# Optimization experiments

Measured on AMD Instinct MI355X. Metric: run time of the kernel, lower is better.

## Reference

```python
import jax, jax.numpy as jnp
import numpy as np

H = 256      # hidden_size (hardcoded by view([-1,1,256]) in the torch source)
V = 50257    # output_size / vocab
L = 50       # max_length


def gru_cell(x, h, w_ih, w_hh, b_ih, b_hh):
    """PyTorch GRUCell semantics. x, h: [H]; w_*: [3H, H]; b_*: [3H]."""
    gi = w_ih @ x + b_ih
    gh = w_hh @ h + b_hh
    gi_r, gi_z, gi_n = jnp.split(gi, 3)
    gh_r, gh_z, gh_n = jnp.split(gh, 3)
    r = jax.nn.sigmoid(gi_r + gh_r)
    z = jax.nn.sigmoid(gi_z + gh_z)
    n = jnp.tanh(gi_n + r * gh_n)
    return (1.0 - z) * n + z * h


def setup_inputs() -> dict:
    key = jax.random.key(0)
    ks = jax.random.split(key, 24)
    p = lambda k, shape: (0.02 * jax.random.normal(k, shape)).astype(jnp.float32)
    d = {}
    d["token"] = jax.random.randint(ks[0], (1,), 0, V)
    d["hidden"] = jax.random.normal(ks[1], (1, 1, H), dtype=jnp.float32)
    d["encoder_outputs"] = jax.random.normal(ks[2], (L, H), dtype=jnp.float32)
    d["emb"] = p(ks[3], (V, H))
    d["attn_W"] = p(ks[4], (L, 2 * H)); d["attn_b"] = jnp.zeros((L,), jnp.float32)
    d["comb_W"] = p(ks[5], (H, 2 * H)); d["comb_b"] = jnp.zeros((H,), jnp.float32)
    # bidirectional GRU: forward (f) and reverse (b) direction weights
    d["w_ih_f"] = p(ks[6], (3 * H, H)); d["w_hh_f"] = p(ks[7], (3 * H, H))
    d["b_ih_f"] = jnp.zeros((3 * H,), jnp.float32); d["b_hh_f"] = jnp.zeros((3 * H,), jnp.float32)
    d["w_ih_b"] = p(ks[8], (3 * H, H)); d["w_hh_b"] = p(ks[9], (3 * H, H))
    d["b_ih_b"] = jnp.zeros((3 * H,), jnp.float32); d["b_hh_b"] = jnp.zeros((3 * H,), jnp.float32)
    # second (unidirectional) GRU
    d["w_ih_g"] = p(ks[10], (3 * H, H)); d["w_hh_g"] = p(ks[11], (3 * H, H))
    d["b_ih_g"] = jnp.zeros((3 * H,), jnp.float32); d["b_hh_g"] = jnp.zeros((3 * H,), jnp.float32)
    d["out_W"] = p(ks[12], (V, H)); d["out_b"] = jnp.zeros((V,), jnp.float32)
    return d


def reference(token, hidden, encoder_outputs, emb, attn_W, attn_b, comb_W, comb_b,
              w_ih_f, w_hh_f, b_ih_f, b_hh_f, w_ih_b, w_hh_b, b_ih_b, b_hh_b,
              w_ih_g, w_hh_g, b_ih_g, b_hh_g, out_W, out_b):
    # dropout is treated as identity (eval mode)
    e = emb[token[0]]                       # [H] embedded token
    h0 = hidden[0, 0]                       # [H]
    # attention weights over encoder positions
    aw = jax.nn.softmax(jax.nn.relu(attn_W @ jnp.concatenate([e, h0]) + attn_b))  # [L]
    applied = aw @ encoder_outputs          # [H]
    x = jax.nn.relu(comb_W @ jnp.concatenate([e, applied]) + comb_b)              # [H]
    # bidirectional GRU, seq_len=1: both directions see the same step, init hidden = h0
    hf = gru_cell(x, h0, w_ih_f, w_hh_f, b_ih_f, b_hh_f)
    hb = gru_cell(x, h0, w_ih_b, w_hh_b, b_ih_b, b_hh_b)
    hm = 0.5 * (hf + hb)                    # torch.mean(bihidden, dim=0)
    # bioutput (1,1,512) viewed as (2,1,256) -> second GRU runs 2 steps
    h1 = gru_cell(hf, hm, w_ih_g, w_hh_g, b_ih_g, b_hh_g)
    h2 = gru_cell(hb, h1, w_ih_g, w_hh_g, b_ih_g, b_hh_g)
    logp = jax.nn.log_softmax(out_W @ h1 + out_b)  # output[0] = first timestep = h1
    return (logp[None, :], h2[None, None, :], aw[None, :])
```

## Files before the change

### kernel.cpp

```cpp
#include <hip/hip_runtime.h>
#include <math.h>

#define H 256
#define L 50
#define V 50257
#define LOGIT_BLKS 786
#define ROWS_PER_WAVE 16
#define FINAL_BLKS 197
#define GRU2_BLKS 64

__device__ __forceinline__ float dot4(float4 a, float4 b) {
    return a.x * b.x + a.y * b.y + a.z * b.z + a.w * b.w;
}

__device__ __forceinline__ float wave_reduce_sum(float v) {
#pragma unroll
    for (int m = 32; m >= 1; m >>= 1) v += __shfl_xor(v, m, 64);
    return v;
}

__device__ __forceinline__ float wave_reduce_max(float v) {
#pragma unroll
    for (int m = 32; m >= 1; m >>= 1) v = fmaxf(v, __shfl_xor(v, m, 64));
    return v;
}

__device__ __forceinline__ float sigmoidf(float x) { return 1.0f / (1.0f + __expf(-x)); }

__device__ __forceinline__ void ms_push(float& m, float& s, float x) {
    float mn = fmaxf(m, x);
    s = s * __expf(m - mn) + __expf(x - mn);
    m = mn;
}
__device__ __forceinline__ void ms_merge(float& m, float& s, float om, float os) {
    float M = fmaxf(m, om);
    float a = (m == -INFINITY) ? 0.f : s * __expf(m - M);
    float c = (om == -INFINITY) ? 0.f : os * __expf(om - M);
    m = M; s = a + c;
}

__device__ __forceinline__ void gru_wave(
    int j, int lane, float4 xv, float4 hv, float hj,
    const float* __restrict__ w_ih, const float* __restrict__ w_hh,
    const float* __restrict__ b_ih, const float* __restrict__ b_hh,
    float* __restrict__ outp)
{
    float gi[3], gh[3];
#pragma unroll
    for (int k = 0; k < 3; ++k) {
        int row = k * H + j;
        const float4* wi4 = (const float4*)(w_ih + (size_t)row * H);
        const float4* wh4 = (const float4*)(w_hh + (size_t)row * H);
        gi[k] = wave_reduce_sum(dot4(wi4[lane], xv)) + b_ih[row];
        gh[k] = wave_reduce_sum(dot4(wh4[lane], hv)) + b_hh[row];
    }
    if (lane == 0) {
        float r = sigmoidf(gi[0] + gh[0]);
        float z = sigmoidf(gi[1] + gh[1]);
        float n = tanhf(gi[2] + r * gh[2]);
        outp[j] = (1.f - z) * n + z * hj;
    }
}

__global__ __launch_bounds__(256) void k_comb(
    const int* __restrict__ token, const float* __restrict__ hidden,
    const float* __restrict__ emb, const float* __restrict__ attn_W,
    const float* __restrict__ attn_b, const float* __restrict__ enc,
    const float* __restrict__ comb_W, const float* __restrict__ comb_b,
    float* __restrict__ ws_x, float* __restrict__ out_aw)
{
    __shared__ __align__(16) float s_cat[2 * H];
    __shared__ float s_aw[64];
    int t = threadIdx.x, wid = t >> 6, lane = t & 63;
    int tok = token[0];
    s_cat[t] = emb[(size_t)tok * H + t];
    s_cat[H + t] = hidden[t];
    __syncthreads();
    const float4* c4 = (const float4*)s_cat;
    float4 cA = c4[lane];
    float4 cB = c4[lane + 64];
    for (int r = wid; r < L; r += 4) {
        const float4* W4 = (const float4*)(attn_W + (size_t)r * 2 * H);
        float acc = dot4(W4[lane], cA) + dot4(W4[lane + 64], cB);
        acc = wave_reduce_sum(acc);
        if (lane == 0) s_aw[r] = fmaxf(acc + attn_b[r], 0.f);
    }
    __syncthreads();
    if (t < 64) {
        float v = (t < L) ? s_aw[t] : -INFINITY;
        float mx = wave_reduce_max(v);
        float e = (t < L) ? __expf(v - mx) : 0.f;
        float ssum = wave_reduce_sum(e);
        if (t < L) {
            float aw = e / ssum;
            s_aw[t] = aw;
            if (blockIdx.x == 0) out_aw[t] = aw;
        }
    }
    __syncthreads();
    float app = 0.f;
    for (int l = 0; l < L; ++l) app += s_aw[l] * enc[l * H + t];
    s_cat[H + t] = app;
    __syncthreads();
    int row = blockIdx.x * 4 + wid;
    const float4* Wc = (const float4*)(comb_W + (size_t)row * 2 * H);
    float4 cB2 = c4[lane + 64];
    float acc = dot4(Wc[lane], cA) + dot4(Wc[lane + 64], cB2);
    acc = wave_reduce_sum(acc);
    if (lane == 0) ws_x[row] = fmaxf(acc + comb_b[row], 0.f);
}

__global__ __launch_bounds__(256) void k_gru_fb(
    const float* __restrict__ ws_x, const float* __restrict__ hidden,
    const float* __restrict__ w_ih_f, const float* __restrict__ w_hh_f,
    const float* __restrict__ b_ih_f, const float* __restrict__ b_hh_f,
    const float* __restrict__ w_ih_b, const float* __restrict__ w_hh_b,
    const float* __restrict__ b_ih_b, const float* __restrict__ b_hh_b,
    float* __restrict__ ws_hf, float* __restrict__ ws_hb)
{
    int t = threadIdx.x, wid = t >> 6, lane = t & 63;
    int g = blockIdx.x * 4 + wid;
    int dir = g >> 8, j = g & 255;
    gru_wave(j, lane, ((const float4*)ws_x)[lane], ((const float4*)hidden)[lane],
             hidden[j],
             dir ? w_ih_b : w_ih_f, dir ? w_hh_b : w_hh_f,
             dir ? b_ih_b : b_ih_f, dir ? b_hh_b : b_hh_f,
             dir ? ws_hb : ws_hf);
}

__global__ __launch_bounds__(256) void k_gru(
    const float* __restrict__ xvec, const float* __restrict__ ha,
    const float* __restrict__ hb,
    const float* __restrict__ w_ih, const float* __restrict__ w_hh,
    const float* __restrict__ b_ih, const float* __restrict__ b_hh,
    float* __restrict__ outp)
{
    int t = threadIdx.x, wid = t >> 6, lane = t & 63;
    int j = blockIdx.x * 4 + wid;
    float4 xv = ((const float4*)xvec)[lane];
    float4 hv = ((const float4*)ha)[lane];
    float hj;
    if (hb) {
        float4 bv = ((const float4*)hb)[lane];
        hv = make_float4(0.5f * (hv.x + bv.x), 0.5f * (hv.y + bv.y),
                         0.5f * (hv.z + bv.z), 0.5f * (hv.w + bv.w));
        hj = 0.5f * (ha[j] + hb[j]);
    } else {
        hj = ha[j];
    }
    gru_wave(j, lane, xv, hv, hj, w_ih, w_hh, b_ih, b_hh, outp);
}

__global__ __launch_bounds__(256) void k_logits(
    const float* __restrict__ out_W, const float* __restrict__ out_b,
    const float* __restrict__ h1, float* __restrict__ logits,
    float* __restrict__ part_m, float* __restrict__ part_s)
{
    __shared__ float s_m4[4], s_s4[4];
    int t = threadIdx.x, wid = t >> 6, lane = t & 63;
    float4 hv = ((const float4*)h1)[lane];
    int base = (blockIdx.x * 4 + wid) * ROWS_PER_WAVE;
    float m = -INFINITY, s = 0.f;
#pragma unroll 1
    for (int k = 0; k < ROWS_PER_WAVE; k += 2) {
        int v = base + k;
        if (v >= V) break;
        const float4* W0 = (const float4*)(out_W + (size_t)v * H);
        float4 a0 = W0[lane];
        bool has2 = (v + 1 < V);
        float4 a1 = has2 ? ((const float4*)(out_W + (size_t)(v + 1) * H))[lane]
                         : make_float4(0.f, 0.f, 0.f, 0.f);
        float x0 = wave_reduce_sum(dot4(a0, hv)) + out_b[v];
        float x1 = wave_reduce_sum(dot4(a1, hv));
        if (lane == 0) logits[v] = x0;
        ms_push(m, s, x0);
        if (has2) {
            x1 += out_b[v + 1];
            if (lane == 0) logits[v + 1] = x1;
            ms_push(m, s, x1);
        }
    }
    if (lane == 0) { s_m4[wid] = m; s_s4[wid] = s; }
    __syncthreads();
    if (t == 0) {
        float M = s_m4[0], S = s_s4[0];
#pragma unroll
        for (int q = 1; q < 4; ++q) ms_merge(M, S, s_m4[q], s_s4[q]);
        part_m[blockIdx.x] = M; part_s[blockIdx.x] = S;
    }
}

__global__ __launch_bounds__(256) void k_final(
    const float* __restrict__ part_m, const float* __restrict__ part_s,
    float* __restrict__ logits,
    const float* __restrict__ h1, const float* __restrict__ hb,
    const float* __restrict__ w_ih_g, const float* __restrict__ w_hh_g,
    const float* __restrict__ b_ih_g, const float* __restrict__ b_hh_g,
    float* __restrict__ out_h2)
{
    int t = threadIdx.x, wid = t >> 6, lane = t & 63;
    if (blockIdx.x >= FINAL_BLKS) {
        int j = (blockIdx.x - FINAL_BLKS) * 4 + wid;
        gru_wave(j, lane, ((const float4*)hb)[lane], ((const float4*)h1)[lane],
                 h1[j], w_ih_g, w_hh_g, b_ih_g, b_hh_g, out_h2);
        return;
    }
    __shared__ float s_m4[4], s_s4[4];
    __shared__ float s_bcast;
    float m = -INFINITY, s = 0.f;
    for (int idx = t; idx < LOGIT_BLKS; idx += 256)
        ms_merge(m, s, part_m[idx], part_s[idx]);
#pragma unroll
    for (int d = 32; d >= 1; d >>= 1) {
        float om = __shfl_xor(m, d, 64);
        float os = __shfl_xor(s, d, 64);
        ms_merge(m, s, om, os);
    }
    if (lane == 0) { s_m4[wid] = m; s_s4[wid] = s; }
    __syncthreads();
    if (t == 0) {
        float M = s_m4[0], S = s_s4[0];
#pragma unroll
        for (int q = 1; q < 4; ++q) ms_merge(M, S, s_m4[q], s_s4[q]);
        s_bcast = M + logf(S);
    }
    __syncthreads();
    float lse = s_bcast;
    int i = blockIdx.x * 256 + t;
    if (i < V) logits[i] -= lse;
}

extern "C" void kernel_launch(void* const* d_in, const int* in_sizes, int n_in,
                              void* d_out, int out_size, void* d_ws, size_t ws_size,
                              hipStream_t stream)
{
    const int*   token  = (const int*)d_in[0];
    const float* hidden = (const float*)d_in[1];
    const float* enc    = (const float*)d_in[2];
    const float* emb    = (const float*)d_in[3];
    const float* attn_W = (const float*)d_in[4];
    const float* attn_b = (const float*)d_in[5];
    const float* comb_W = (const float*)d_in[6];
    const float* comb_b = (const float*)d_in[7];
    const float* w_ih_f = (const float*)d_in[8];
    const float* w_hh_f = (const float*)d_in[9];
    const float* b_ih_f = (const float*)d_in[10];
    const float* b_hh_f = (const float*)d_in[11];
    const float* w_ih_b = (const float*)d_in[12];
    const float* w_hh_b = (const float*)d_in[13];
    const float* b_ih_b = (const float*)d_in[14];
    const float* b_hh_b = (const float*)d_in[15];
    const float* w_ih_g = (const float*)d_in[16];
    const float* w_hh_g = (const float*)d_in[17];
    const float* b_ih_g = (const float*)d_in[18];
    const float* b_hh_g = (const float*)d_in[19];
    const float* out_W  = (const float*)d_in[20];
    const float* out_b  = (const float*)d_in[21];

    float* out = (float*)d_out;
    float* ws  = (float*)d_ws;
    float* ws_x      = ws;
    float* ws_hf     = ws + 256;
    float* ws_hb     = ws + 512;
    float* ws_h1     = ws + 768;
    float* part_m    = ws + 1024;
    float* part_s    = ws + 1856;

    k_comb<<<64, 256, 0, stream>>>(token, hidden, emb, attn_W, attn_b, enc,
                                   comb_W, comb_b, ws_x, out + V + H);
    k_gru_fb<<<128, 256, 0, stream>>>(ws_x, hidden,
                                      w_ih_f, w_hh_f, b_ih_f, b_hh_f,
                                      w_ih_b, w_hh_b, b_ih_b, b_hh_b,
                                      ws_hf, ws_hb);
    k_gru<<<64, 256, 0, stream>>>(ws_hf, ws_hf, ws_hb,
                                  w_ih_g, w_hh_g, b_ih_g, b_hh_g, ws_h1);
    k_logits<<<LOGIT_BLKS, 256, 0, stream>>>(out_W, out_b, ws_h1, out,
                                             part_m, part_s);
    k_final<<<FINAL_BLKS + GRU2_BLKS, 256, 0, stream>>>(
        part_m, part_s, out, ws_h1, ws_hb,
        w_ih_g, w_hh_g, b_ih_g, b_hh_g, out + V);
}
```

Before: 182.3 us.

## Fuse attention, GRU stages and logits into one kernel with flag-based inter-block sync

Merges the combine, bidirectional GRU, first second-GRU step and logits kernels into a single launch. Block ranges are assigned to each stage, and dependent blocks spin on per-block release/acquire flags in the workspace instead of waiting for kernel boundaries. Logit blocks prefetch most of their out_W rows into registers before waiting for h1, so the weight streaming overlaps the serial GRU chain. Flags are set to a fixed magic value and never cleared, so if the workspace persists across calls, later calls can read stale intermediates. The spin-waits also depend on producer blocks being resident together with the waiting blocks.

New measurement: 447.2 us. 145% more time.

```diff
diff --git a/kernel.cpp b/kernel.cpp
--- a/kernel.cpp
+++ b/kernel.cpp
@@ -4,10 +4,23 @@
 #define H 256
 #define L 50
 #define V 50257
-#define LOGIT_BLKS 786
-#define ROWS_PER_WAVE 16
+#define MAGIC 0x5F3C7A19u
+
+#define COMB_NB 64
+#define FB_B0   64
+#define FB_NB   128
+#define G1_B0   192
+#define G1_NB   64
+#define SW_B0   256
+#define SW_NB   640
+#define NBLK1   (SW_B0 + SW_NB)
+#define ROWS    20
+#define HOLD    12
+#define NPART   SW_NB
+
 #define FINAL_BLKS 197
-#define GRU2_BLKS 64
+#define H2_NB      64
+#define NBLK2      (FINAL_BLKS + H2_NB)
 
 __device__ __forceinline__ float dot4(float4 a, float4 b) {
     return a.x * b.x + a.y * b.y + a.z * b.z + a.w * b.w;
@@ -26,6 +39,19 @@
 }
 
 __device__ __forceinline__ float sigmoidf(float x) { return 1.0f / (1.0f + __expf(-x)); }
+
+__device__ __forceinline__ void st_flag(unsigned* p, unsigned v) {
+    __hip_atomic_store(p, v, __ATOMIC_RELEASE, __HIP_MEMORY_SCOPE_AGENT);
+}
+__device__ __forceinline__ unsigned ld_flag(const unsigned* p) {
+    return __hip_atomic_load(p, __ATOMIC_ACQUIRE, __HIP_MEMORY_SCOPE_AGENT);
+}
+__device__ __forceinline__ void st_f(float* p, float v) {
+    __hip_atomic_store(p, v, __ATOMIC_RELAXED, __HIP_MEMORY_SCOPE_AGENT);
+}
+__device__ __forceinline__ float ld_f(const float* p) {
+    return __hip_atomic_load(p, __ATOMIC_RELAXED, __HIP_MEMORY_SCOPE_AGENT);
+}
 
 __device__ __forceinline__ void ms_push(float& m, float& s, float x) {
     float mn = fmaxf(m, x);
@@ -58,135 +84,171 @@
         float r = sigmoidf(gi[0] + gh[0]);
         float z = sigmoidf(gi[1] + gh[1]);
         float n = tanhf(gi[2] + r * gh[2]);
-        outp[j] = (1.f - z) * n + z * hj;
-    }
-}
-
-__global__ __launch_bounds__(256) void k_comb(
+        st_f(outp + j, (1.f - z) * n + z * hj);
+    }
+}
+
+__global__ __launch_bounds__(256, 4) void k_fused(
     const int* __restrict__ token, const float* __restrict__ hidden,
-    const float* __restrict__ emb, const float* __restrict__ attn_W,
-    const float* __restrict__ attn_b, const float* __restrict__ enc,
+    const float* __restrict__ enc, const float* __restrict__ emb,
+    const float* __restrict__ attn_W, const float* __restrict__ attn_b,
     const float* __restrict__ comb_W, const float* __restrict__ comb_b,
-    float* __restrict__ ws_x, float* __restrict__ out_aw)
-{
-    __shared__ __align__(16) float s_cat[2 * H];
-    __shared__ float s_aw[64];
-    int t = threadIdx.x, wid = t >> 6, lane = t & 63;
-    int tok = token[0];
-    s_cat[t] = emb[(size_t)tok * H + t];
-    s_cat[H + t] = hidden[t];
-    __syncthreads();
-    const float4* c4 = (const float4*)s_cat;
-    float4 cA = c4[lane];
-    float4 cB = c4[lane + 64];
-    for (int r = wid; r < L; r += 4) {
-        const float4* W4 = (const float4*)(attn_W + (size_t)r * 2 * H);
-        float acc = dot4(W4[lane], cA) + dot4(W4[lane + 64], cB);
-        acc = wave_reduce_sum(acc);
-        if (lane == 0) s_aw[r] = fmaxf(acc + attn_b[r], 0.f);
-    }
-    __syncthreads();
-    if (t < 64) {
-        float v = (t < L) ? s_aw[t] : -INFINITY;
-        float mx = wave_reduce_max(v);
-        float e = (t < L) ? __expf(v - mx) : 0.f;
-        float ssum = wave_reduce_sum(e);
-        if (t < L) {
-            float aw = e / ssum;
-            s_aw[t] = aw;
-            if (blockIdx.x == 0) out_aw[t] = aw;
-        }
-    }
-    __syncthreads();
-    float app = 0.f;
-    for (int l = 0; l < L; ++l) app += s_aw[l] * enc[l * H + t];
-    s_cat[H + t] = app;
-    __syncthreads();
-    int row = blockIdx.x * 4 + wid;
-    const float4* Wc = (const float4*)(comb_W + (size_t)row * 2 * H);
-    float4 cB2 = c4[lane + 64];
-    float acc = dot4(Wc[lane], cA) + dot4(Wc[lane + 64], cB2);
-    acc = wave_reduce_sum(acc);
-    if (lane == 0) ws_x[row] = fmaxf(acc + comb_b[row], 0.f);
-}
-
-__global__ __launch_bounds__(256) void k_gru_fb(
-    const float* __restrict__ ws_x, const float* __restrict__ hidden,
     const float* __restrict__ w_ih_f, const float* __restrict__ w_hh_f,
     const float* __restrict__ b_ih_f, const float* __restrict__ b_hh_f,
     const float* __restrict__ w_ih_b, const float* __restrict__ w_hh_b,
     const float* __restrict__ b_ih_b, const float* __restrict__ b_hh_b,
-    float* __restrict__ ws_hf, float* __restrict__ ws_hb)
+    const float* __restrict__ w_ih_g, const float* __restrict__ w_hh_g,
+    const float* __restrict__ b_ih_g, const float* __restrict__ b_hh_g,
+    const float* __restrict__ out_W, const float* __restrict__ out_b,
+    float* __restrict__ out_logp, float* __restrict__ out_aw,
+    float* __restrict__ ws_x, float* __restrict__ ws_hf,
+    float* __restrict__ ws_hb, float* __restrict__ ws_h1,
+    float* __restrict__ part_m, float* __restrict__ part_s,
+    unsigned* __restrict__ flags)
 {
+    __shared__ float smem[576];
     int t = threadIdx.x, wid = t >> 6, lane = t & 63;
-    int g = blockIdx.x * 4 + wid;
-    int dir = g >> 8, j = g & 255;
-    gru_wave(j, lane, ((const float4*)ws_x)[lane], ((const float4*)hidden)[lane],
-             hidden[j],
-             dir ? w_ih_b : w_ih_f, dir ? w_hh_b : w_hh_f,
-             dir ? b_ih_b : b_ih_f, dir ? b_hh_b : b_hh_f,
-             dir ? ws_hb : ws_hf);
-}
-
-__global__ __launch_bounds__(256) void k_gru(
-    const float* __restrict__ xvec, const float* __restrict__ ha,
-    const float* __restrict__ hb,
-    const float* __restrict__ w_ih, const float* __restrict__ w_hh,
-    const float* __restrict__ b_ih, const float* __restrict__ b_hh,
-    float* __restrict__ outp)
-{
-    int t = threadIdx.x, wid = t >> 6, lane = t & 63;
-    int j = blockIdx.x * 4 + wid;
-    float4 xv = ((const float4*)xvec)[lane];
-    float4 hv = ((const float4*)ha)[lane];
-    float hj;
-    if (hb) {
-        float4 bv = ((const float4*)hb)[lane];
-        hv = make_float4(0.5f * (hv.x + bv.x), 0.5f * (hv.y + bv.y),
-                         0.5f * (hv.z + bv.z), 0.5f * (hv.w + bv.w));
-        hj = 0.5f * (ha[j] + hb[j]);
-    } else {
-        hj = ha[j];
-    }
-    gru_wave(j, lane, xv, hv, hj, w_ih, w_hh, b_ih, b_hh, outp);
-}
-
-__global__ __launch_bounds__(256) void k_logits(
-    const float* __restrict__ out_W, const float* __restrict__ out_b,
-    const float* __restrict__ h1, float* __restrict__ logits,
-    float* __restrict__ part_m, float* __restrict__ part_s)
-{
-    __shared__ float s_m4[4], s_s4[4];
-    int t = threadIdx.x, wid = t >> 6, lane = t & 63;
-    float4 hv = ((const float4*)h1)[lane];
-    int base = (blockIdx.x * 4 + wid) * ROWS_PER_WAVE;
-    float m = -INFINITY, s = 0.f;
-#pragma unroll 1
-    for (int k = 0; k < ROWS_PER_WAVE; k += 2) {
-        int v = base + k;
-        if (v >= V) break;
-        const float4* W0 = (const float4*)(out_W + (size_t)v * H);
-        float4 a0 = W0[lane];
-        bool has2 = (v + 1 < V);
-        float4 a1 = has2 ? ((const float4*)(out_W + (size_t)(v + 1) * H))[lane]
-                         : make_float4(0.f, 0.f, 0.f, 0.f);
-        float x0 = wave_reduce_sum(dot4(a0, hv)) + out_b[v];
-        float x1 = wave_reduce_sum(dot4(a1, hv));
-        if (lane == 0) logits[v] = x0;
-        ms_push(m, s, x0);
-        if (has2) {
-            x1 += out_b[v + 1];
-            if (lane == 0) logits[v + 1] = x1;
-            ms_push(m, s, x1);
-        }
-    }
-    if (lane == 0) { s_m4[wid] = m; s_s4[wid] = s; }
-    __syncthreads();
-    if (t == 0) {
-        float M = s_m4[0], S = s_s4[0];
-#pragma unroll
-        for (int q = 1; q < 4; ++q) ms_merge(M, S, s_m4[q], s_s4[q]);
-        part_m[blockIdx.x] = M; part_s[blockIdx.x] = S;
+    int b = blockIdx.x;
+    unsigned* fx  = flags;
+    unsigned* ffb = flags + 64;
+    unsigned* fh1 = flags + 192;
+
+    if (b >= SW_B0) {
+        int sid = b - SW_B0;
+        int base = (sid * 4 + wid) * ROWS;
+        float4 hld[HOLD];
+#pragma unroll
+        for (int k = 0; k < HOLD; ++k) {
+            int vc = base + k; if (vc > V - 1) vc = V - 1;
+            hld[k] = ((const float4*)(out_W + (size_t)vc * H))[lane];
+        }
+        __builtin_amdgcn_sched_barrier(0);
+        float* s_h1 = smem;
+        float* s_m4 = smem + 256;
+        float* s_s4 = smem + 260;
+        if (t < 64) {
+            while (ld_flag(fh1 + t) != MAGIC) __builtin_amdgcn_s_sleep(1);
+        }
+        __syncthreads();
+        s_h1[t] = ld_f(ws_h1 + t);
+        __syncthreads();
+        float4 hv = ((const float4*)s_h1)[lane];
+        float m = -INFINITY, s = 0.f;
+#pragma unroll
+        for (int k = 0; k < HOLD; ++k) {
+            int v = base + k;
+            float x0 = wave_reduce_sum(dot4(hld[k], hv));
+            if (v < V) {
+                x0 += out_b[v];
+                if (lane == 0) out_logp[v] = x0;
+                ms_push(m, s, x0);
+            }
+        }
+#pragma unroll 2
+        for (int k = HOLD; k < ROWS; ++k) {
+            int v = base + k; int vc = (v > V - 1) ? V - 1 : v;
+            float4 a = ((const float4*)(out_W + (size_t)vc * H))[lane];
+            float x0 = wave_reduce_sum(dot4(a, hv));
+            if (v < V) {
+                x0 += out_b[v];
+                if (lane == 0) out_logp[v] = x0;
+                ms_push(m, s, x0);
+            }
+        }
+        if (lane == 0) { s_m4[wid] = m; s_s4[wid] = s; }
+        __syncthreads();
+        if (t == 0) {
+            float M = s_m4[0], S = s_s4[0];
+#pragma unroll
+            for (int q = 1; q < 4; ++q) ms_merge(M, S, s_m4[q], s_s4[q]);
+            part_m[sid] = M; part_s[sid] = S;
+        }
+        return;
+    }
+
+    if (b < COMB_NB) {
+        float* s_cat = smem;
+        float* s_aw  = smem + 512;
+        int tok = token[0];
+        s_cat[t] = emb[(size_t)tok * H + t];
+        s_cat[H + t] = hidden[t];
+        __syncthreads();
+        const float4* c4 = (const float4*)s_cat;
+        float4 cA = c4[lane];
+        float4 cB = c4[lane + 64];
+        for (int r = wid; r < L; r += 4) {
+            const float4* W4 = (const float4*)(attn_W + (size_t)r * 2 * H);
+            float acc = dot4(W4[lane], cA) + dot4(W4[lane + 64], cB);
+            acc = wave_reduce_sum(acc);
+            if (lane == 0) s_aw[r] = fmaxf(acc + attn_b[r], 0.f);
+        }
+        __syncthreads();
+        if (t < 64) {
+            float v = (t < L) ? s_aw[t] : -INFINITY;
+            float mx = wave_reduce_max(v);
+            float e = (t < L) ? __expf(v - mx) : 0.f;
+            float ssum = wave_reduce_sum(e);
+            if (t < L) {
+                float aw = e / ssum;
+                s_aw[t] = aw;
+                if (b == 0) out_aw[t] = aw;
+            }
+        }
+        __syncthreads();
+        float app = 0.f;
+        for (int l = 0; l < L; ++l) app += s_aw[l] * enc[l * H + t];
+        s_cat[H + t] = app;
+        __syncthreads();
+        int row = b * 4 + wid;
+        const float4* Wc = (const float4*)(comb_W + (size_t)row * 2 * H);
+        float acc = dot4(Wc[lane], cA) + dot4(Wc[lane + 64], c4[lane + 64]);
+        acc = wave_reduce_sum(acc);
+        if (lane == 0) st_f(ws_x + row, fmaxf(acc + comb_b[row], 0.f));
+        __syncthreads();
+        if (t == 0) { __threadfence(); st_flag(fx + b, MAGIC); }
+        return;
+    }
+
+    if (b < G1_B0) {
+        float* s_x = smem;
+        if (t < 64) {
+            while (ld_flag(fx + t) != MAGIC) __builtin_amdgcn_s_sleep(1);
+        }
+        __syncthreads();
+        s_x[t] = ld_f(ws_x + t);
+        __syncthreads();
+        int g = (b - FB_B0) * 4 + wid;
+        int dir = g >> 8, j = g & 255;
+        gru_wave(j, lane, ((const float4*)s_x)[lane], ((const float4*)hidden)[lane],
+                 hidden[j],
+                 dir ? w_ih_b : w_ih_f, dir ? w_hh_b : w_hh_f,
+                 dir ? b_ih_b : b_ih_f, dir ? b_hh_b : b_hh_f,
+                 dir ? ws_hb : ws_hf);
+        __syncthreads();
+        if (t == 0) { __threadfence(); st_flag(ffb + (b - FB_B0), MAGIC); }
+        return;
+    }
+
+    {
+        float* s_hf = smem;
+        float* s_hb = smem + 256;
+        if (t < 128) {
+            while (ld_flag(ffb + t) != MAGIC) __builtin_amdgcn_s_sleep(1);
+        }
+        __syncthreads();
+        s_hf[t] = ld_f(ws_hf + t);
+        s_hb[t] = ld_f(ws_hb + t);
+        __syncthreads();
+        int j = (b - G1_B0) * 4 + wid;
+        float4 fv = ((const float4*)s_hf)[lane];
+        float4 bv = ((const float4*)s_hb)[lane];
+        float4 hv = make_float4(0.5f * (fv.x + bv.x), 0.5f * (fv.y + bv.y),
+                                0.5f * (fv.z + bv.z), 0.5f * (fv.w + bv.w));
+        float hj = 0.5f * (s_hf[j] + s_hb[j]);
+        gru_wave(j, lane, fv, hv, hj, w_ih_g, w_hh_g, b_ih_g, b_hh_g, ws_h1);
+        __syncthreads();
+        if (t == 0) { __threadfence(); st_flag(fh1 + (b - G1_B0), MAGIC); }
+        return;
     }
 }
 
@@ -208,7 +270,7 @@
     __shared__ float s_m4[4], s_s4[4];
     __shared__ float s_bcast;
     float m = -INFINITY, s = 0.f;
-    for (int idx = t; idx < LOGIT_BLKS; idx += 256)
+    for (int idx = t; idx < NPART; idx += 256)
         ms_merge(m, s, part_m[idx], part_s[idx]);
 #pragma unroll
     for (int d = 32; d >= 1; d >>= 1) {
@@ -259,24 +321,21 @@
 
     float* out = (float*)d_out;
     float* ws  = (float*)d_ws;
-    float* ws_x      = ws;
-    float* ws_hf     = ws + 256;
-    float* ws_hb     = ws + 512;
-    float* ws_h1     = ws + 768;
-    float* part_m    = ws + 1024;
-    float* part_s    = ws + 1856;
-
-    k_comb<<<64, 256, 0, stream>>>(token, hidden, emb, attn_W, attn_b, enc,
-                                   comb_W, comb_b, ws_x, out + V + H);
-    k_gru_fb<<<128, 256, 0, stream>>>(ws_x, hidden,
-                                      w_ih_f, w_hh_f, b_ih_f, b_hh_f,
-                                      w_ih_b, w_hh_b, b_ih_b, b_hh_b,
-                                      ws_hf, ws_hb);
-    k_gru<<<64, 256, 0, stream>>>(ws_hf, ws_hf, ws_hb,
-                                  w_ih_g, w_hh_g, b_ih_g, b_hh_g, ws_h1);
-    k_logits<<<LOGIT_BLKS, 256, 0, stream>>>(out_W, out_b, ws_h1, out,
-                                             part_m, part_s);
-    k_final<<<FINAL_BLKS + GRU2_BLKS, 256, 0, stream>>>(
+    float* ws_x   = ws;
+    float* ws_hf  = ws + 256;
+    float* ws_hb  = ws + 512;
+    float* ws_h1  = ws + 768;
+    float* part_m = ws + 1024;
+    float* part_s = ws + 1664;
+    unsigned* flags = (unsigned*)(ws + 2304);
+
+    k_fused<<<NBLK1, 256, 0, stream>>>(
+        token, hidden, enc, emb, attn_W, attn_b, comb_W, comb_b,
+        w_ih_f, w_hh_f, b_ih_f, b_hh_f, w_ih_b, w_hh_b, b_ih_b, b_hh_b,
+        w_ih_g, w_hh_g, b_ih_g, b_hh_g, out_W, out_b,
+        out, out + V + H,
+        ws_x, ws_hf, ws_hb, ws_h1, part_m, part_s, flags);
+    k_final<<<NBLK2, 256, 0, stream>>>(
         part_m, part_s, out, ws_h1, ws_hb,
         w_ih_g, w_hh_g, b_ih_g, b_hh_g, out + V);
 }
```
